# Kernel tuning notes

Measured on AMD Instinct MI355X. Metric: run time of the kernel, lower is better.

## Reference

```python
import jax, jax.numpy as jnp
import numpy as np

D_MODEL = 1024
NUM_HEADS = 16
D_K = D_MODEL // NUM_HEADS
B, T = 4, 2048


def setup_inputs() -> dict:
    key = jax.random.key(0)
    ks = jax.random.split(key, 12)
    s = 0.02
    inp = {
        "query": jax.random.normal(ks[0], (B, T, D_MODEL), jnp.float32),
        "key": jax.random.normal(ks[1], (B, T, D_MODEL), jnp.float32),
        "value": jax.random.normal(ks[2], (B, T, D_MODEL), jnp.float32),
        "mask": jnp.tril(jnp.ones((T, T), jnp.int32))[None, None],  # [1,1,T,T] causal
        "Wq": jax.random.normal(ks[3], (D_MODEL, D_MODEL), jnp.float32) * s,
        "bq": jnp.zeros((D_MODEL,), jnp.float32),
        "Wk": jax.random.normal(ks[4], (D_MODEL, D_MODEL), jnp.float32) * s,
        "bk": jnp.zeros((D_MODEL,), jnp.float32),
        "Wv": jax.random.normal(ks[5], (D_MODEL, D_MODEL), jnp.float32) * s,
        "bv": jnp.zeros((D_MODEL,), jnp.float32),
        "Wo": jax.random.normal(ks[6], (D_MODEL, D_MODEL), jnp.float32) * s,
        "bo": jnp.zeros((D_MODEL,), jnp.float32),
    }
    return inp


def reference(query, key, value, mask, Wq, bq, Wk, bk, Wv, bv, Wo, bo):
    def split_heads(x):
        # [B,T,D] -> [B,H,T,Dk]
        return x.reshape(B, T, NUM_HEADS, D_K).transpose(0, 2, 1, 3)

    q = split_heads(query @ Wq.T + bq)
    k = split_heads(key @ Wk.T + bk)
    v = split_heads(value @ Wv.T + bv)

    scale = jnp.sqrt(jnp.asarray(D_K, q.dtype))
    scores = jnp.einsum("bhqd,bhkd->bhqk", q, k) / scale  # [B,H,T,T]
    scores = jnp.where(mask == 0, jnp.asarray(-1e9, scores.dtype), scores)
    attn = jax.nn.softmax(scores, axis=-1)
    out = jnp.einsum("bhqk,bhkd->bhqd", attn, v)
    out = out.transpose(0, 2, 1, 3).reshape(B, T, D_MODEL)
    return out @ Wo.T + bo
```

## Files before the change

### kernel.cpp

```cpp
#include <hip/hip_runtime.h>
#include <hip/hip_bf16.h>

#define D_MODEL 1024
#define NHEADS  16
#define DK      64
#define BATCH   4
#define SEQ     2048
#define M_TOT   (BATCH * SEQ)

typedef __attribute__((ext_vector_type(8)))  __bf16 bf16x8;
typedef __attribute__((ext_vector_type(4)))  float  f32x4;
typedef __attribute__((ext_vector_type(16))) float  f32x16;
typedef unsigned short ushort_t;

static __device__ __forceinline__ unsigned int f2bf(float f) {
    union { float f; unsigned int i; } v; v.f = f;
    unsigned int x = v.i;
    return (x + 0x7fffu + ((x >> 16) & 1u)) >> 16;
}

static __device__ __forceinline__ void gl16(const void* g, void* lds_generic) {
    __attribute__((address_space(1))) void* gp =
        (__attribute__((address_space(1))) void*)(unsigned long long)g;
    __attribute__((address_space(3))) void* lp =
        (__attribute__((address_space(3))) void*)(unsigned int)(unsigned long long)lds_generic;
    __builtin_amdgcn_global_load_lds(gp, lp, 16, 0, 0);
}

__global__ __launch_bounds__(256) void cvt_in3(
    const float* __restrict__ i0, const float* __restrict__ i1,
    const float* __restrict__ i2,
    ushort_t* __restrict__ o0, ushort_t* __restrict__ o1,
    ushort_t* __restrict__ o2, int n8)
{
    const float* in; ushort_t* out;
    switch (blockIdx.y) {
        case 0: in = i0; out = o0; break;
        case 1: in = i1; out = o1; break;
        default: in = i2; out = o2; break;
    }
    int i = blockIdx.x * blockDim.x + threadIdx.x;
    if (i >= n8) return;
    const float4* p = (const float4*)in + (size_t)i * 2;
    float4 a = p[0], b = p[1];
    uint4 o;
    o.x = f2bf(a.x) | (f2bf(a.y) << 16);
    o.y = f2bf(a.z) | (f2bf(a.w) << 16);
    o.z = f2bf(b.x) | (f2bf(b.y) << 16);
    o.w = f2bf(b.z) | (f2bf(b.w) << 16);
    *((uint4*)out + i) = o;
}

__global__ __launch_bounds__(256) void cvt_w4(
    const float* __restrict__ w0, const float* __restrict__ w1,
    const float* __restrict__ w2, const float* __restrict__ w3,
    ushort_t* __restrict__ o0, ushort_t* __restrict__ o1,
    ushort_t* __restrict__ o2, ushort_t* __restrict__ o3, int n8)
{
    const float* w; ushort_t* o;
    switch (blockIdx.y) {
        case 0: w = w0; o = o0; break;
        case 1: w = w1; o = o1; break;
        case 2: w = w2; o = o2; break;
        default: w = w3; o = o3; break;
    }
    int i = blockIdx.x * blockDim.x + threadIdx.x;
    if (i >= n8) return;
    const float4* p = (const float4*)w + (size_t)i * 2;
    float4 a = p[0], b = p[1];
    uint4 u;
    u.x = f2bf(a.x) | (f2bf(a.y) << 16);
    u.y = f2bf(a.z) | (f2bf(a.w) << 16);
    u.z = f2bf(b.x) | (f2bf(b.y) << 16);
    u.w = f2bf(b.z) | (f2bf(b.w) << 16);
    *((uint4*)o + i) = u;
}

__global__ __launch_bounds__(256) void gemm_nt_bias(
    const ushort_t* __restrict__ A0, const ushort_t* __restrict__ A1,
    const ushort_t* __restrict__ A2,
    const ushort_t* __restrict__ B0, const ushort_t* __restrict__ B1,
    const ushort_t* __restrict__ B2,
    const float* __restrict__ b0, const float* __restrict__ b1,
    const float* __restrict__ b2,
    void* __restrict__ O0, void* __restrict__ O1, void* __restrict__ O2,
    int mode)
{
    const int z = blockIdx.z;
    const ushort_t* A  = (z == 0) ? A0 : (z == 1) ? A1 : A2;
    const ushort_t* Bt = (z == 0) ? B0 : (z == 1) ? B1 : B2;
    const float* bias  = (z == 0) ? b0 : (z == 1) ? b1 : b2;
    void* OutV         = (z == 0) ? O0 : (z == 1) ? O1 : O2;
    const float oscale = (mode == 1 && z == 0) ? 0.18033688f : 1.0f;

    __shared__ ushort_t sA[2][128 * 64];
    __shared__ ushort_t sB[2][128 * 64];
    const int K    = 1024;
    const int tid  = threadIdx.x;
    const int lane = tid & 63;
    const int wave = tid >> 6;

    const int flat = (int)blockIdx.x + 8 * (int)blockIdx.y;
    const int nf   = (flat & 7) * 64 + (flat >> 3);
    const int m0   = (nf >> 3) * 128;
    const int n0   = (nf & 7) * 128;

    const int wrow = (wave >> 1) * 64;
    const int wcol = (wave & 1) * 64;
    const int l15  = lane & 15;
    const int quad = lane >> 4;
    const int swz  = l15 & 7;

    size_t aoffs[4], boffs[4];
#pragma unroll
    for (int i = 0; i < 4; i++) {
        int c = tid + 256 * i;
        int row = c >> 3;
        int ch  = (c & 7) ^ (row & 7);
        aoffs[i] = (size_t)(m0 + row) * K + ch * 8;
        boffs[i] = (size_t)(n0 + row) * K + ch * 8;
    }

    f32x4 acc[4][4];
#pragma unroll
    for (int i = 0; i < 4; i++)
#pragma unroll
        for (int j = 0; j < 4; j++)
#pragma unroll
            for (int r = 0; r < 4; r++) acc[i][j][r] = 0.0f;

    auto stage = [&](int buf, int kt) {
#pragma unroll
        for (int i = 0; i < 4; i++) {
            int c = tid + 256 * i;
            gl16(A + aoffs[i] + kt, &sA[buf][c * 8]);
            gl16(Bt + boffs[i] + kt, &sB[buf][c * 8]);
        }
    };

    stage(0, 0);
    asm volatile("s_waitcnt vmcnt(0)");
    __syncthreads();
    int cur = 0;

    for (int kt = 0; kt < K; kt += 64) {
        if (kt + 64 < K) stage(cur ^ 1, kt + 64);

#pragma unroll
        for (int kk = 0; kk < 2; kk++) {
            bf16x8 afr[4], bfr[4];
            const int chp = ((kk * 4 + quad) ^ swz) * 8;
#pragma unroll
            for (int i = 0; i < 4; i++)
                afr[i] = *(const bf16x8*)(&sA[cur][(wrow + i * 16 + l15) * 64 + chp]);
#pragma unroll
            for (int j = 0; j < 4; j++)
                bfr[j] = *(const bf16x8*)(&sB[cur][(wcol + j * 16 + l15) * 64 + chp]);
#pragma unroll
            for (int i = 0; i < 4; i++)
#pragma unroll
                for (int j = 0; j < 4; j++)
                    acc[i][j] = __builtin_amdgcn_mfma_f32_16x16x32_bf16(
                        afr[i], bfr[j], acc[i][j], 0, 0, 0);
        }

        asm volatile("s_waitcnt vmcnt(0)");
        __syncthreads();
        cur ^= 1;
    }

    if (mode == 1 && z == 2) {
#pragma unroll
        for (int j = 0; j < 4; j++) {
            int col  = n0 + wcol + j * 16 + l15;
            float bv = bias[col];
            int h = col >> 6, dk = col & 63;
#pragma unroll
            for (int i = 0; i < 4; i++) {
                int row0 = m0 + wrow + i * 16 + quad * 4;
                int b = row0 >> 11, t0 = row0 & 2047;
                ushort_t pk[4];
#pragma unroll
                for (int r = 0; r < 4; r++)
                    pk[r] = (ushort_t)f2bf(acc[i][j][r] + bv);
                *(uint2*)&((ushort_t*)OutV)[((size_t)(b * 16 + h) * 64 + dk) * SEQ + t0] =
                    *(const uint2*)pk;
            }
        }
        return;
    }

#pragma unroll
    for (int j = 0; j < 4; j++) {
        int col  = n0 + wcol + j * 16 + l15;
        float bv = bias[col];
#pragma unroll
        for (int i = 0; i < 4; i++) {
#pragma unroll
            for (int r = 0; r < 4; r++) {
                int row = m0 + wrow + i * 16 + quad * 4 + r;
                float o = (acc[i][j][r] + bv) * oscale;
                if (mode == 0) {
                    ((ushort_t*)OutV)[(size_t)row * 1024 + col] = (ushort_t)f2bf(o);
                } else if (mode == 1) {
                    int b = row >> 11, t = row & 2047;
                    int h = col >> 6,  dk = col & 63;
                    ((ushort_t*)OutV)[((size_t)(b * 16 + h) * 2048 + t) * 64 + dk] =
                        (ushort_t)f2bf(o);
                } else {
                    ((float*)OutV)[(size_t)row * 1024 + col] = o;
                }
            }
        }
    }
}

__global__ __launch_bounds__(256, 2) void attn_causal(
    const ushort_t* __restrict__ Q,
    const ushort_t* __restrict__ Km,
    const ushort_t* __restrict__ Vt,
    ushort_t* __restrict__ O)
{
    __shared__ ushort_t sK[2][64 * 64];
    __shared__ ushort_t sVt[2][64 * 64];

    const int tid  = threadIdx.x;
    const int lane = tid & 63;
    const int wave = tid >> 6;
    const int l31  = lane & 31;
    const int hi   = lane >> 5;
    const int bh   = blockIdx.x;
    const int pi   = blockIdx.y;
    const int usplit = 15 - pi;
    const size_t base = (size_t)bh * SEQ * 64;

    size_t ksrc[2], vsrc[2];
#pragma unroll
    for (int i = 0; i < 2; i++) {
        int c  = tid + 256 * i;
        int kr = c >> 3, kc = (c & 7) ^ (kr & 7);
        ksrc[i] = base + (size_t)kr * 64 + kc * 8;
        int vr = c >> 3, vc = (c & 7) ^ (vr & 7);
        vsrc[i] = base + (size_t)vr * SEQ + vc * 8;
    }

    bf16x8 qfr[4];
    f32x16 oacc[2];
    float  ls[4];

    auto zacc = [&]() {
#pragma unroll
        for (int j = 0; j < 2; j++)
#pragma unroll
            for (int r = 0; r < 16; r++) oacc[j][r] = 0.0f;
#pragma unroll
        for (int r = 0; r < 4; r++) ls[r] = 0.0f;
    };

    auto loadQ = [&](int qtile) {
        const size_t qrow = base + (size_t)(qtile * 128 + wave * 32 + l31) * 64;
#pragma unroll
        for (int kk = 0; kk < 4; kk++)
            qfr[kk] = *(const bf16x8*)&Q[qrow + kk * 16 + hi * 8];
    };

    auto stage = [&](int buf, int s) {
        const size_t ko = (size_t)s * 64 * 64;
        const size_t vo = (size_t)s * 64;
#pragma unroll
        for (int i = 0; i < 2; i++) {
            int c = tid + 256 * i;
            gl16(Km + ksrc[i] + ko, &sK[buf][c * 8]);
            gl16(Vt + vsrc[i] + vo, &sVt[buf][c * 8]);
        }
    };

    auto compute = [&](int cur, int s64, int qtile) {
        const ushort_t* kb_ = &sK[cur][0];
        const ushort_t* vb_ = &sVt[cur][0];
        const int kv0   = s64 * 64;
        const int qgmin = qtile * 128 + wave * 32;
        const int qg    = qgmin + l31;

        f32x16 sacc[2];
#pragma unroll
        for (int b = 0; b < 2; b++) {
            if (kv0 + b * 32 > qgmin + 31) continue;
#pragma unroll
            for (int r = 0; r < 16; r++) sacc[b][r] = 0.0f;
            const int krow = b * 32 + l31;
            const int ksw  = krow & 7;
            __builtin_amdgcn_s_setprio(1);
#pragma unroll
            for (int kk = 0; kk < 4; kk++) {
                bf16x8 afr = *(const bf16x8*)&kb_[krow * 64 + (((kk * 2 + hi) ^ ksw) * 8)];
                sacc[b] = __builtin_amdgcn_mfma_f32_32x32x16_bf16(afr, qfr[kk], sacc[b], 0, 0, 0);
            }
            __builtin_amdgcn_s_setprio(0);
        }

#pragma unroll
        for (int b = 0; b < 2; b++) {
            if (kv0 + b * 32 > qgmin + 31) continue;
            const bool maskb = (kv0 + b * 32 + 31) > qgmin;

            float p[16];
#pragma unroll
            for (int r = 0; r < 16; r++) {
                float v = sacc[b][r];
                if (maskb) {
                    int kvg = kv0 + b * 32 + (r & 3) + 8 * (r >> 2) + 4 * hi;
                    if (kvg > qg) v = -INFINITY;
                }
                float e = __builtin_amdgcn_exp2f(v);
                p[r] = e;
                ls[r & 3] += e;
            }

            unsigned w[8];
#pragma unroll
            for (int t = 0; t < 4; t++) {
                asm("v_cvt_pk_bf16_f32 %0, %1, %2"
                    : "=v"(w[2 * t]) : "v"(p[4 * t]), "v"(p[4 * t + 1]));
                asm("v_cvt_pk_bf16_f32 %0, %1, %2"
                    : "=v"(w[2 * t + 1]) : "v"(p[4 * t + 2]), "v"(p[4 * t + 3]));
            }

#pragma unroll
            for (int kb = 0; kb < 2; kb++) {
                unsigned aA = w[kb * 4 + 0], bA = w[kb * 4 + 2];
                unsigned aB = w[kb * 4 + 1], bB = w[kb * 4 + 3];
                asm("v_permlane32_swap_b32 %0, %1" : "+v"(aA), "+v"(bA));
                asm("v_permlane32_swap_b32 %0, %1" : "+v"(aB), "+v"(bB));
                union { unsigned u[4]; bf16x8 v8; } fr;
                fr.u[0] = aA; fr.u[1] = aB; fr.u[2] = bA; fr.u[3] = bB;
                __builtin_amdgcn_s_setprio(1);
#pragma unroll
                for (int j = 0; j < 2; j++) {
                    const int vrow = j * 32 + l31;
                    bf16x8 bfr = *(const bf16x8*)&vb_[
                        vrow * 64 + (((b * 4 + kb * 2 + hi) ^ (vrow & 7)) * 8)];
                    oacc[j] = __builtin_amdgcn_mfma_f32_32x32x16_bf16(
                        fr.v8, bfr, oacc[j], 0, 0, 0);
                }
                __builtin_amdgcn_s_setprio(0);
            }
        }
    };

    const int ob = bh >> 4, oh = bh & 15;
    auto epilogue = [&](int qtile) {
        float lsum = (ls[0] + ls[1]) + (ls[2] + ls[3]);
        float tot = lsum + __shfl_xor(lsum, 32);
        float inv = 1.0f / tot;
#pragma unroll
        for (int r = 0; r < 16; r++) {
            int qloc = (r & 3) + 8 * (r >> 2) + 4 * hi;
            float invr = __shfl(inv, qloc);
            int qg2 = qtile * 128 + wave * 32 + qloc;
#pragma unroll
            for (int j = 0; j < 2; j++) {
                O[((size_t)(ob * SEQ) + qg2) * 1024 + oh * 64 + j * 32 + l31] =
                    (ushort_t)f2bf(oacc[j][r] * invr);
            }
        }
    };

    zacc();
    loadQ(usplit);
    int qtile = usplit;
    const int send1 = 2 * usplit + 1;
    stage(0, 0);
    asm volatile("s_waitcnt vmcnt(0)");
    __syncthreads();
    int cur = 0;
    for (int u = 0; u <= 33; ++u) {
        if (u < 33) {
            int un = u + 1;
            int sn = (un <= send1) ? un : (un - send1 - 1);
            stage(cur ^ 1, sn);
        }
        int sc = (u <= send1) ? u : (u - send1 - 1);
        compute(cur, sc, qtile);
        if (u == send1) {
            epilogue(qtile);
            zacc();
            qtile = pi;
            loadQ(pi);
        }
        asm volatile("s_waitcnt vmcnt(0)");
        __syncthreads();
        cur ^= 1;
    }
    epilogue(qtile);
}

extern "C" void kernel_launch(void* const* d_in, const int* in_sizes, int n_in,
                              void* d_out, int out_size, void* d_ws, size_t ws_size,
                              hipStream_t stream) {
    const float* q_in = (const float*)d_in[0];
    const float* k_in = (const float*)d_in[1];
    const float* v_in = (const float*)d_in[2];
    const float* Wq = (const float*)d_in[4];
    const float* bq = (const float*)d_in[5];
    const float* Wk = (const float*)d_in[6];
    const float* bk = (const float*)d_in[7];
    const float* Wv = (const float*)d_in[8];
    const float* bv = (const float*)d_in[9];
    const float* Wo = (const float*)d_in[10];
    const float* bo = (const float*)d_in[11];

    ushort_t* ws = (ushort_t*)d_ws;
    const size_t TEN = (size_t)M_TOT * D_MODEL;
    const size_t WEL = (size_t)D_MODEL * D_MODEL;
    ushort_t* tmp = ws;
    ushort_t* WqB = ws + TEN;
    ushort_t* WkB = WqB + WEL;
    ushort_t* WvB = WkB + WEL;
    ushort_t* WoB = WvB + WEL;
    ushort_t* qw  = WoB + WEL;
    ushort_t* kw  = qw + TEN;
    ushort_t* vw  = kw + TEN;
    ushort_t* ow  = vw + TEN;
    ushort_t* vstage = (ushort_t*)d_out;

    dim3 bb(256);
    const int n8_in = (int)(TEN / 8);
    const int n8_w  = (int)(WEL / 8);

    cvt_w4<<<dim3(n8_w / 256, 4), bb, 0, stream>>>(Wq, Wk, Wv, Wo, WqB, WkB, WvB, WoB, n8_w);
    cvt_in3<<<dim3(n8_in / 256, 3), bb, 0, stream>>>(q_in, k_in, v_in, tmp, ow, vstage, n8_in);

    gemm_nt_bias<<<dim3(D_MODEL / 128, M_TOT / 128, 3), bb, 0, stream>>>(
        tmp, ow, vstage, WqB, WkB, WvB, bq, bk, bv, qw, kw, vw, 1);

    attn_causal<<<dim3(BATCH * NHEADS, 8), bb, 0, stream>>>(qw, kw, vw, ow);

    gemm_nt_bias<<<dim3(D_MODEL / 128, M_TOT / 128, 1), bb, 0, stream>>>(
        ow, ow, ow, WoB, WoB, WoB, bo, bo, bo, d_out, d_out, d_out, 2);
}
```

Measured before the change: 311.0 us.

## Replace paired causal q-tile scheduling with one q-tile per block

Before, each block handled two query tiles (15-pi and pi) so that every block did the same amount of causal work. Now each block handles a single query tile, and the grid doubles to 16 tiles per batch-head, with heavy tiles scheduled first. This gives 1024 blocks instead of 512 and a simpler loop with no mid-loop epilogue or reload. The cost is uneven per-block work, which relies on the hardware scheduler to fill the tail with short blocks.

```diff
diff --git a/kernel.cpp b/kernel.cpp
--- a/kernel.cpp
+++ b/kernel.cpp
@@ -230,8 +230,7 @@
     const int l31  = lane & 31;
     const int hi   = lane >> 5;
     const int bh   = blockIdx.x;
-    const int pi   = blockIdx.y;
-    const int usplit = 15 - pi;
+    const int qtile = 15 - (int)blockIdx.y;
     const size_t base = (size_t)bh * SEQ * 64;
 
     size_t ksrc[2], vsrc[2];
@@ -248,21 +247,19 @@
     f32x16 oacc[2];
     float  ls[4];
 
-    auto zacc = [&]() {
-#pragma unroll
-        for (int j = 0; j < 2; j++)
-#pragma unroll
-            for (int r = 0; r < 16; r++) oacc[j][r] = 0.0f;
-#pragma unroll
-        for (int r = 0; r < 4; r++) ls[r] = 0.0f;
-    };
-
-    auto loadQ = [&](int qtile) {
+#pragma unroll
+    for (int j = 0; j < 2; j++)
+#pragma unroll
+        for (int r = 0; r < 16; r++) oacc[j][r] = 0.0f;
+#pragma unroll
+    for (int r = 0; r < 4; r++) ls[r] = 0.0f;
+
+    {
         const size_t qrow = base + (size_t)(qtile * 128 + wave * 32 + l31) * 64;
 #pragma unroll
         for (int kk = 0; kk < 4; kk++)
             qfr[kk] = *(const bf16x8*)&Q[qrow + kk * 16 + hi * 8];
-    };
+    }
 
     auto stage = [&](int buf, int s) {
         const size_t ko = (size_t)s * 64 * 64;
@@ -275,7 +272,7 @@
         }
     };
 
-    auto compute = [&](int cur, int s64, int qtile) {
+    auto compute = [&](int cur, int s64) {
         const ushort_t* kb_ = &sK[cur][0];
         const ushort_t* vb_ = &sVt[cur][0];
         const int kv0   = s64 * 64;
@@ -348,8 +345,21 @@
         }
     };
 
+    const int send = 2 * qtile + 1;
+    stage(0, 0);
+    asm volatile("s_waitcnt vmcnt(0)");
+    __syncthreads();
+    int cur = 0;
+    for (int u = 0; u <= send; ++u) {
+        if (u < send) stage(cur ^ 1, u + 1);
+        compute(cur, u);
+        asm volatile("s_waitcnt vmcnt(0)");
+        __syncthreads();
+        cur ^= 1;
+    }
+
     const int ob = bh >> 4, oh = bh & 15;
-    auto epilogue = [&](int qtile) {
+    {
         float lsum = (ls[0] + ls[1]) + (ls[2] + ls[3]);
         float tot = lsum + __shfl_xor(lsum, 32);
         float inv = 1.0f / tot;
@@ -364,35 +374,7 @@
                     (ushort_t)f2bf(oacc[j][r] * invr);
             }
         }
-    };
-
-    zacc();
-    loadQ(usplit);
-    int qtile = usplit;
-    const int send1 = 2 * usplit + 1;
-    stage(0, 0);
-    asm volatile("s_waitcnt vmcnt(0)");
-    __syncthreads();
-    int cur = 0;
-    for (int u = 0; u <= 33; ++u) {
-        if (u < 33) {
-            int un = u + 1;
-            int sn = (un <= send1) ? un : (un - send1 - 1);
-            stage(cur ^ 1, sn);
-        }
-        int sc = (u <= send1) ? u : (u - send1 - 1);
-        compute(cur, sc, qtile);
-        if (u == send1) {
-            epilogue(qtile);
-            zacc();
-            qtile = pi;
-            loadQ(pi);
-        }
-        asm volatile("s_waitcnt vmcnt(0)");
-        __syncthreads();
-        cur ^= 1;
-    }
-    epilogue(qtile);
+    }
 }
 
 extern "C" void kernel_launch(void* const* d_in, const int* in_sizes, int n_in,
@@ -434,7 +416,7 @@
     gemm_nt_bias<<<dim3(D_MODEL / 128, M_TOT / 128, 3), bb, 0, stream>>>(
         tmp, ow, vstage, WqB, WkB, WvB, bq, bk, bv, qw, kw, vw, 1);
 
-    attn_causal<<<dim3(BATCH * NHEADS, 8), bb, 0, stream>>>(qw, kw, vw, ow);
+    attn_causal<<<dim3(BATCH * NHEADS, 16), bb, 0, stream>>>(qw, kw, vw, ow);
 
     gemm_nt_bias<<<dim3(D_MODEL / 128, M_TOT / 128, 1), bb, 0, stream>>>(
         ow, ow, ow, WoB, WoB, WoB, bo, bo, bo, d_out, d_out, d_out, 2);
```

Result: slower. 320.4 us (+3.0%).
